# Optimization experiments

Measured on AMD Instinct MI355X. Metric: run time of the kernel, lower is better.

The kernel has to match this reference:

```python
import jax, jax.numpy as jnp
import numpy as np

N, D, F, E, K = 8192, 1024, 4096, 8, 2


def setup_inputs() -> dict:
    key = jax.random.key(0)
    ks = jax.random.split(key, 4)
    x = jax.random.normal(ks[0], (N, D), dtype=jnp.float32)
    Wg = jax.random.normal(ks[1], (D, E), dtype=jnp.float32) * 0.02
    W1 = jax.random.normal(ks[2], (E, D, F), dtype=jnp.float32) * 0.02
    b1 = jnp.zeros((E, F), dtype=jnp.float32)
    W2 = jax.random.normal(ks[3], (E, F, D), dtype=jnp.float32) * 0.02
    b2 = jnp.zeros((E, D), dtype=jnp.float32)
    return {"x": x, "Wg": Wg, "W1": W1, "b1": b1, "W2": W2, "b2": b2}


def reference(x, Wg, W1, b1, W2, b2):
    # Top-k softmax gate (TopKGate): pick K experts per token, renormalize.
    logits = x @ Wg                                        # [N, E]
    probs = jax.nn.softmax(logits, axis=-1)
    gate_vals, expert_idx = jax.lax.top_k(probs, K)        # [N, K]
    gate_w = gate_vals / jnp.sum(gate_vals, axis=-1, keepdims=True)

    # Expert FFN (dispatch/combine math): the torch code sorts tokens by expert
    # id, all-to-alls them to the owning rank, applies the local Expert MLP,
    # and combines back weighted by gate_w. The jit-friendly equivalent is to
    # compute every expert's MLP for all tokens and gather the selected rows.
    h = jax.nn.relu(jnp.einsum('nd,edf->enf', x, W1) + b1[:, None, :])  # [E, N, F]
    o = jnp.einsum('enf,efd->end', h, W2) + b2[:, None, :]               # [E, N, D]

    tok = jnp.arange(x.shape[0])
    sel = o[expert_idx, tok[:, None]]                      # [N, K, D]
    y = jnp.sum(gate_w[..., None] * sel, axis=1)           # [N, D]
    return y
```

## Files before the change

kernel.cpp:

```cpp
#include <hip/hip_runtime.h>

#define N_TOK 8192
#define DIM   1024
#define FFN   4096
#define NEXP  8
#define TOPK  2
#define NENT  (N_TOK * TOPK)
#define MAXM  20

using short8  = __attribute__((ext_vector_type(8))) short;
using floatx4 = __attribute__((ext_vector_type(4))) float;

__device__ __forceinline__ unsigned short f2bf(float f) {
    union { float f; unsigned u; } v; v.f = f;
    unsigned r = v.u + 0x7fffu + ((v.u >> 16) & 1u);
    return (unsigned short)(r >> 16);
}

__device__ __forceinline__ float bf2f(unsigned short s) {
    union { unsigned u; float f; } v; v.u = ((unsigned)s) << 16;
    return v.f;
}

#define GLOAD_LDS16(gptr, lptr) __builtin_amdgcn_global_load_lds( \
    (__attribute__((address_space(1))) void*)(void*)(gptr),       \
    (__attribute__((address_space(3))) void*)(lptr), 16, 0, 0)


__global__ __launch_bounds__(256) void transpose_cvt(const float* __restrict__ in,
                                                     unsigned short* __restrict__ out,
                                                     int R, int C) {
    __shared__ float tile[64][65];
    int e  = blockIdx.z;
    int c0 = blockIdx.x * 64;
    int r0 = blockIdx.y * 64;
    const float* inp = in + (size_t)e * R * C;
    unsigned short* outp = out + (size_t)e * R * C;
    int tid = threadIdx.x;
    int lrow = tid >> 4;
    int lc4  = (tid & 15) * 4;
#pragma unroll
    for (int i = 0; i < 4; i++) {
        int r = i * 16 + lrow;
        float4 v = *(const float4*)&inp[(size_t)(r0 + r) * C + c0 + lc4];
        tile[r][lc4 + 0] = v.x;
        tile[r][lc4 + 1] = v.y;
        tile[r][lc4 + 2] = v.z;
        tile[r][lc4 + 3] = v.w;
    }
    __syncthreads();
    int r4 = (tid & 15) * 4;
#pragma unroll
    for (int i = 0; i < 4; i++) {
        int c = i * 16 + (tid >> 4);
        ushort4 o;
        o.x = f2bf(tile[r4 + 0][c]);
        o.y = f2bf(tile[r4 + 1][c]);
        o.z = f2bf(tile[r4 + 2][c]);
        o.w = f2bf(tile[r4 + 3][c]);
        *(ushort4*)&outp[(size_t)(c0 + c) * R + r0 + r4] = o;
    }
}


__global__ __launch_bounds__(256) void gating_kernel(const float* __restrict__ x,
                                                     const float* __restrict__ wg,
                                                     unsigned short* __restrict__ xb,
                                                     int* __restrict__ topk_e,
                                                     float* __restrict__ topk_w,
                                                     int* __restrict__ counts) {
    int wave = threadIdx.x >> 6, lane = threadIdx.x & 63;
    int t = blockIdx.x * 4 + wave;
    const float* xr = x + (size_t)t * DIM;
    unsigned short* xbr = xb + (size_t)t * DIM;
    float acc[NEXP];
#pragma unroll
    for (int e = 0; e < NEXP; e++) acc[e] = 0.f;
    for (int it = 0; it < DIM / 64; it++) {
        int d = it * 64 + lane;
        float xv = xr[d];
        xbr[d] = f2bf(xv);
        const float4* wr = (const float4*)(wg + d * NEXP);
        float4 w0 = wr[0], w1 = wr[1];
        acc[0] += xv * w0.x; acc[1] += xv * w0.y; acc[2] += xv * w0.z; acc[3] += xv * w0.w;
        acc[4] += xv * w1.x; acc[5] += xv * w1.y; acc[6] += xv * w1.z; acc[7] += xv * w1.w;
    }
#pragma unroll
    for (int e = 0; e < NEXP; e++) {
#pragma unroll
        for (int off = 32; off > 0; off >>= 1) acc[e] += __shfl_xor(acc[e], off);
    }
    if (lane == 0) {
        int e1 = 0; float l1 = acc[0];
        for (int e = 1; e < NEXP; e++) if (acc[e] > l1) { l1 = acc[e]; e1 = e; }
        int e2 = -1; float l2 = -3.4e38f;
        for (int e = 0; e < NEXP; e++) if (e != e1 && acc[e] > l2) { l2 = acc[e]; e2 = e; }
        float w1v = 1.f / (1.f + expf(l2 - l1));
        topk_e[t * 2]     = e1;  topk_e[t * 2 + 1] = e2;
        topk_w[t * 2]     = w1v; topk_w[t * 2 + 1] = 1.f - w1v;
        atomicAdd(&counts[e1], 1);
        atomicAdd(&counts[e2], 1);
    }
}

__global__ __launch_bounds__(256) void scatter_kernel(const int* __restrict__ topk_e,
                                                      const float* __restrict__ topk_w,
                                                      const int* __restrict__ counts,
                                                      int* __restrict__ offs,
                                                      int* __restrict__ cursors,
                                                      int* __restrict__ entry_token,
                                                      int* __restrict__ entry_pos) {
    int off_[NEXP]; int s = 0;
#pragma unroll
    for (int e = 0; e < NEXP; e++) { off_[e] = s; s += counts[e]; }
    if (blockIdx.x == 0 && threadIdx.x == 0) {
#pragma unroll
        for (int e = 0; e < NEXP; e++) offs[e] = off_[e];
        offs[NEXP] = s;
    }
    int t = blockIdx.x * 256 + threadIdx.x;
#pragma unroll
    for (int k = 0; k < TOPK; k++) {
        int e = topk_e[t * 2 + k];
        int pos = off_[e] + atomicAdd(&cursors[e], 1);
        entry_token[pos] = t;
        entry_pos[t * 2 + k] = pos;
    }
}


__global__ __launch_bounds__(256, 3) void gemm1_kernel(
    const unsigned short* __restrict__ xb,
    const unsigned short* __restrict__ w1t,
    const float* __restrict__ b1,
    const int* __restrict__ offs,
    const int* __restrict__ entry_token,
    unsigned short* __restrict__ h)
{
    int bid   = blockIdx.x;
    int xcd   = bid & 7;
    int inner = bid >> 3;
    int gq    = inner / MAXM;
    int mt    = inner - gq * MAXM;
    int g     = gq * 8 + xcd;
    int e     = g >> 5;
    int nt    = g & 31;
    int base = offs[e];
    int cnt  = offs[e + 1] - base;
    int m0   = mt * 128;
    if (m0 >= cnt) return;
    int f0   = nt * 128;

    __shared__ unsigned short As[2][128 * 32];
    __shared__ unsigned short Bs[2][128 * 32];
    __shared__ int toks[128];

    int tid = threadIdx.x;
    if (tid < 128) {
        int r = m0 + tid;
        toks[tid] = entry_token[base + (r < cnt ? r : 0)];
    }
    __syncthreads();

    int wave = tid >> 6, lane = tid & 63;
    int wm = (wave >> 1) * 64, wn = (wave & 1) * 64;

    int lr = lane >> 2, sl = lane & 3;
    int g0 = (sl ^ ((lr >> 1) & 3)) * 8;
    const unsigned short* aG[2];
    const unsigned short* bG[2];
    int ldsOff[2];
#pragma unroll
    for (int c = 0; c < 2; c++) {
        int row = wave * 32 + c * 16 + lr;
        aG[c] = xb + (size_t)toks[row] * DIM + g0;
        bG[c] = w1t + ((size_t)e * FFN + f0 + row) * DIM + g0;
        ldsOff[c] = (wave * 32 + c * 16) * 32;
    }

    floatx4 acc[4][4];
#pragma unroll
    for (int i = 0; i < 4; i++)
#pragma unroll
        for (int j = 0; j < 4; j++) acc[i][j] = (floatx4)0.f;

    int quad = lane >> 4, rm = lane & 15;
    int slf  = (quad ^ ((rm >> 1) & 3)) * 8;
    int arow = (wm + rm) * 32;
    int brow = (wn + rm) * 32;

#pragma unroll
    for (int c = 0; c < 2; c++) {
        GLOAD_LDS16(aG[c], &As[0][ldsOff[c]]);
        GLOAD_LDS16(bG[c], &Bs[0][ldsOff[c]]);
        aG[c] += 32; bG[c] += 32;
    }

    int cur = 0;
    for (int kk = 0; kk < DIM / 32; kk++) {
        __syncthreads();
        short8 af[4], bfr[4];
#pragma unroll
        for (int mi = 0; mi < 4; mi++) af[mi] = *(const short8*)&As[cur][arow + mi * 512 + slf];
#pragma unroll
        for (int ni = 0; ni < 4; ni++) bfr[ni] = *(const short8*)&Bs[cur][brow + ni * 512 + slf];
        if (kk + 1 < DIM / 32) {
            int nxt = cur ^ 1;
#pragma unroll
            for (int c = 0; c < 2; c++) {
                GLOAD_LDS16(aG[c], &As[nxt][ldsOff[c]]);
                GLOAD_LDS16(bG[c], &Bs[nxt][ldsOff[c]]);
                aG[c] += 32; bG[c] += 32;
            }
        }
#pragma unroll
        for (int mi = 0; mi < 4; mi++)
#pragma unroll
            for (int ni = 0; ni < 4; ni++)
                acc[mi][ni] = __builtin_amdgcn_mfma_f32_16x16x32_bf16(af[mi], bfr[ni], acc[mi][ni], 0, 0, 0);
        cur ^= 1;
    }

#pragma unroll
    for (int mi = 0; mi < 4; mi++) {
        int mbase = wm + mi * 16 + quad * 4;
#pragma unroll
        for (int ni = 0; ni < 4; ni++) {
            int f = f0 + wn + ni * 16 + rm;
            float bias = b1[e * FFN + f];
            floatx4 v = acc[mi][ni];
#pragma unroll
            for (int r = 0; r < 4; r++) {
                int row = m0 + mbase + r;
                if (row < cnt) {
                    float t = v[r] + bias;
                    t = t > 0.f ? t : 0.f;
                    h[(size_t)(base + row) * FFN + f] = f2bf(t);
                }
            }
        }
    }
}


__global__ __launch_bounds__(256, 3) void gemm2_kernel(
    const unsigned short* __restrict__ h,
    const unsigned short* __restrict__ w2t,
    const float* __restrict__ b2,
    const int* __restrict__ offs,
    unsigned short* __restrict__ o)
{
    int bid  = blockIdx.x;
    int e    = bid & 7;
    int grp  = bid % (8 * MAXM);
    int mt   = grp >> 3;
    int nt   = bid / (8 * MAXM);
    int base = offs[e];
    int cnt  = offs[e + 1] - base;
    int m0   = mt * 128;
    if (m0 >= cnt) return;
    int n0   = nt * 128;

    __shared__ unsigned short As[2][128 * 32];
    __shared__ unsigned short Bs[2][128 * 32];

    int tid = threadIdx.x;
    int wave = tid >> 6, lane = tid & 63;
    int wm = (wave >> 1) * 64, wn = (wave & 1) * 64;

    int lr = lane >> 2, sl = lane & 3;
    int g0 = (sl ^ ((lr >> 1) & 3)) * 8;
    const unsigned short* aG[2];
    const unsigned short* bG[2];
    int ldsOff[2];
#pragma unroll
    for (int c = 0; c < 2; c++) {
        int row = wave * 32 + c * 16 + lr;
        aG[c] = h + (size_t)(base + m0 + row) * FFN + g0;
        bG[c] = w2t + ((size_t)e * DIM + n0 + row) * FFN + g0;
        ldsOff[c] = (wave * 32 + c * 16) * 32;
    }

    floatx4 acc[4][4];
#pragma unroll
    for (int i = 0; i < 4; i++)
#pragma unroll
        for (int j = 0; j < 4; j++) acc[i][j] = (floatx4)0.f;

    int quad = lane >> 4, rm = lane & 15;
    int slf  = (quad ^ ((rm >> 1) & 3)) * 8;
    int arow = (wm + rm) * 32;
    int brow = (wn + rm) * 32;

#pragma unroll
    for (int c = 0; c < 2; c++) {
        GLOAD_LDS16(aG[c], &As[0][ldsOff[c]]);
        GLOAD_LDS16(bG[c], &Bs[0][ldsOff[c]]);
        aG[c] += 32; bG[c] += 32;
    }

    int cur = 0;
    for (int kk = 0; kk < FFN / 32; kk++) {
        __syncthreads();
        short8 af[4], bfr[4];
#pragma unroll
        for (int mi = 0; mi < 4; mi++) af[mi] = *(const short8*)&As[cur][arow + mi * 512 + slf];
#pragma unroll
        for (int ni = 0; ni < 4; ni++) bfr[ni] = *(const short8*)&Bs[cur][brow + ni * 512 + slf];
        if (kk + 1 < FFN / 32) {
            int nxt = cur ^ 1;
#pragma unroll
            for (int c = 0; c < 2; c++) {
                GLOAD_LDS16(aG[c], &As[nxt][ldsOff[c]]);
                GLOAD_LDS16(bG[c], &Bs[nxt][ldsOff[c]]);
                aG[c] += 32; bG[c] += 32;
            }
        }
#pragma unroll
        for (int mi = 0; mi < 4; mi++)
#pragma unroll
            for (int ni = 0; ni < 4; ni++)
                acc[mi][ni] = __builtin_amdgcn_mfma_f32_16x16x32_bf16(af[mi], bfr[ni], acc[mi][ni], 0, 0, 0);
        cur ^= 1;
    }

#pragma unroll
    for (int mi = 0; mi < 4; mi++) {
        int mbase = wm + mi * 16 + quad * 4;
#pragma unroll
        for (int ni = 0; ni < 4; ni++) {
            int n = n0 + wn + ni * 16 + rm;
            float bias = b2[e * DIM + n];
            floatx4 v = acc[mi][ni];
#pragma unroll
            for (int r = 0; r < 4; r++) {
                int row = m0 + mbase + r;
                if (row < cnt)
                    o[(size_t)(base + row) * DIM + n] = f2bf(v[r] + bias);
            }
        }
    }
}


__global__ __launch_bounds__(256) void combine_kernel(const unsigned short* __restrict__ o,
                                                      const int* __restrict__ entry_pos,
                                                      const float* __restrict__ topk_w,
                                                      float* __restrict__ y) {
    int t = blockIdx.x;
    int d = threadIdx.x * 4;
    int p0 = entry_pos[t * 2], p1 = entry_pos[t * 2 + 1];
    float w0 = topk_w[t * 2], w1 = topk_w[t * 2 + 1];
    ushort4 a = *(const ushort4*)&o[(size_t)p0 * DIM + d];
    ushort4 b = *(const ushort4*)&o[(size_t)p1 * DIM + d];
    float4 r;
    r.x = w0 * bf2f(a.x) + w1 * bf2f(b.x);
    r.y = w0 * bf2f(a.y) + w1 * bf2f(b.y);
    r.z = w0 * bf2f(a.z) + w1 * bf2f(b.z);
    r.w = w0 * bf2f(a.w) + w1 * bf2f(b.w);
    *(float4*)&y[(size_t)t * DIM + d] = r;
}


extern "C" void kernel_launch(void* const* d_in, const int* in_sizes, int n_in,
                              void* d_out, int out_size, void* d_ws, size_t ws_size,
                              hipStream_t stream) {
    const float* x  = (const float*)d_in[0];
    const float* Wg = (const float*)d_in[1];
    const float* W1 = (const float*)d_in[2];
    const float* b1 = (const float*)d_in[3];
    const float* W2 = (const float*)d_in[4];
    const float* b2 = (const float*)d_in[5];
    float* y = (float*)d_out;

    char* p = (char*)d_ws;
    unsigned short* xb  = (unsigned short*)p; p += (size_t)N_TOK * DIM * 2;
    unsigned short* w1t = (unsigned short*)p; p += (size_t)NEXP * DIM * FFN * 2;
    unsigned short* w2t = (unsigned short*)p; p += (size_t)NEXP * DIM * FFN * 2;
    unsigned short* h   = (unsigned short*)p; p += (size_t)(NENT + 128) * FFN * 2;
    int*   topk_e      = (int*)p;   p += (size_t)N_TOK * TOPK * 4;
    float* topk_w      = (float*)p; p += (size_t)N_TOK * TOPK * 4;
    int*   entry_token = (int*)p;   p += (size_t)NENT * 4;
    int*   entry_pos   = (int*)p;   p += (size_t)NENT * 4;
    int*   counts      = (int*)p;   p += NEXP * 4;
    int*   cursors     = (int*)p;   p += NEXP * 4;
    int*   offs        = (int*)p;   p += (NEXP + 1) * 4;

    unsigned short* o = w1t;

    hipMemsetAsync(counts, 0, NEXP * 4 * 2, stream);

    transpose_cvt<<<dim3(FFN / 64, DIM / 64, NEXP), 256, 0, stream>>>(W1, w1t, DIM, FFN);
    transpose_cvt<<<dim3(DIM / 64, FFN / 64, NEXP), 256, 0, stream>>>(W2, w2t, FFN, DIM);
    gating_kernel<<<N_TOK / 4, 256, 0, stream>>>(x, Wg, xb, topk_e, topk_w, counts);
    scatter_kernel<<<N_TOK / 256, 256, 0, stream>>>(topk_e, topk_w, counts, offs, cursors, entry_token, entry_pos);
    gemm1_kernel<<<NEXP * MAXM * (FFN / 128), 256, 0, stream>>>(xb, w1t, b1, offs, entry_token, h);
    gemm2_kernel<<<NEXP * MAXM * (DIM / 128), 256, 0, stream>>>(h, w2t, b2, offs, o);
    combine_kernel<<<N_TOK, 256, 0, stream>>>(o, entry_pos, topk_w, y);
}
```

Before: 996.0 us.

## Fuse combine into gemm2 epilogue via atomics and merge prep kernels

The weight transposes and the gating kernel are merged into one launch, and the gating loop now uses float4 loads. The combine kernel is removed. gemm2's epilogue instead scales each row by its gate weight and atomically adds it into a zeroed fp32 output, indexed by token. This drops the bf16 intermediate o buffer, its write and read-back, and two launches, at the cost of a memset of y, scattered fp32 atomics, and non-deterministic summation order.

```diff
diff --git a/kernel.cpp b/kernel.cpp
--- a/kernel.cpp
+++ b/kernel.cpp
@@ -17,73 +17,85 @@
     return (unsigned short)(r >> 16);
 }
 
-__device__ __forceinline__ float bf2f(unsigned short s) {
-    union { unsigned u; float f; } v; v.u = ((unsigned)s) << 16;
-    return v.f;
-}
-
 #define GLOAD_LDS16(gptr, lptr) __builtin_amdgcn_global_load_lds( \
     (__attribute__((address_space(1))) void*)(void*)(gptr),       \
     (__attribute__((address_space(3))) void*)(lptr), 16, 0, 0)
 
 
-__global__ __launch_bounds__(256) void transpose_cvt(const float* __restrict__ in,
-                                                     unsigned short* __restrict__ out,
-                                                     int R, int C) {
+__global__ __launch_bounds__(256) void prep_kernel(
+    const float* __restrict__ W1, const float* __restrict__ W2,
+    unsigned short* __restrict__ w1t, unsigned short* __restrict__ w2t,
+    const float* __restrict__ x, const float* __restrict__ wg,
+    unsigned short* __restrict__ xb,
+    int* __restrict__ topk_e, float* __restrict__ topk_w,
+    int* __restrict__ counts)
+{
     __shared__ float tile[64][65];
-    int e  = blockIdx.z;
-    int c0 = blockIdx.x * 64;
-    int r0 = blockIdx.y * 64;
-    const float* inp = in + (size_t)e * R * C;
-    unsigned short* outp = out + (size_t)e * R * C;
+    int bid = blockIdx.x;
     int tid = threadIdx.x;
-    int lrow = tid >> 4;
-    int lc4  = (tid & 15) * 4;
-#pragma unroll
-    for (int i = 0; i < 4; i++) {
-        int r = i * 16 + lrow;
-        float4 v = *(const float4*)&inp[(size_t)(r0 + r) * C + c0 + lc4];
-        tile[r][lc4 + 0] = v.x;
-        tile[r][lc4 + 1] = v.y;
-        tile[r][lc4 + 2] = v.z;
-        tile[r][lc4 + 3] = v.w;
-    }
-    __syncthreads();
-    int r4 = (tid & 15) * 4;
-#pragma unroll
-    for (int i = 0; i < 4; i++) {
-        int c = i * 16 + (tid >> 4);
-        ushort4 o;
-        o.x = f2bf(tile[r4 + 0][c]);
-        o.y = f2bf(tile[r4 + 1][c]);
-        o.z = f2bf(tile[r4 + 2][c]);
-        o.w = f2bf(tile[r4 + 3][c]);
-        *(ushort4*)&outp[(size_t)(c0 + c) * R + r0 + r4] = o;
-    }
-}
-
-
-__global__ __launch_bounds__(256) void gating_kernel(const float* __restrict__ x,
-                                                     const float* __restrict__ wg,
-                                                     unsigned short* __restrict__ xb,
-                                                     int* __restrict__ topk_e,
-                                                     float* __restrict__ topk_w,
-                                                     int* __restrict__ counts) {
-    int wave = threadIdx.x >> 6, lane = threadIdx.x & 63;
-    int t = blockIdx.x * 4 + wave;
+
+    if (bid < 16384) {
+        const float* in; unsigned short* out; int R, C, e, c0, r0;
+        if (bid < 8192) {
+            in = W1; out = w1t; R = DIM; C = FFN;
+            e = bid >> 10; int b = bid & 1023;
+            c0 = (b & 63) * 64; r0 = (b >> 6) * 64;
+        } else {
+            int bb = bid - 8192;
+            in = W2; out = w2t; R = FFN; C = DIM;
+            e = bb >> 10; int b = bb & 1023;
+            c0 = (b & 15) * 64; r0 = (b >> 4) * 64;
+        }
+        const float* inp = in + (size_t)e * DIM * FFN;
+        unsigned short* outp = out + (size_t)e * DIM * FFN;
+        int lrow = tid >> 4;
+        int lc4  = (tid & 15) * 4;
+#pragma unroll
+        for (int i = 0; i < 4; i++) {
+            int r = i * 16 + lrow;
+            float4 v = *(const float4*)&inp[(size_t)(r0 + r) * C + c0 + lc4];
+            tile[r][lc4 + 0] = v.x;
+            tile[r][lc4 + 1] = v.y;
+            tile[r][lc4 + 2] = v.z;
+            tile[r][lc4 + 3] = v.w;
+        }
+        __syncthreads();
+        int r4 = (tid & 15) * 4;
+#pragma unroll
+        for (int i = 0; i < 4; i++) {
+            int c = i * 16 + (tid >> 4);
+            ushort4 o;
+            o.x = f2bf(tile[r4 + 0][c]);
+            o.y = f2bf(tile[r4 + 1][c]);
+            o.z = f2bf(tile[r4 + 2][c]);
+            o.w = f2bf(tile[r4 + 3][c]);
+            *(ushort4*)&outp[(size_t)(c0 + c) * R + r0 + r4] = o;
+        }
+        return;
+    }
+
+    int wave = tid >> 6, lane = tid & 63;
+    int t = (bid - 16384) * 4 + wave;
     const float* xr = x + (size_t)t * DIM;
     unsigned short* xbr = xb + (size_t)t * DIM;
     float acc[NEXP];
 #pragma unroll
     for (int e = 0; e < NEXP; e++) acc[e] = 0.f;
-    for (int it = 0; it < DIM / 64; it++) {
-        int d = it * 64 + lane;
-        float xv = xr[d];
-        xbr[d] = f2bf(xv);
-        const float4* wr = (const float4*)(wg + d * NEXP);
-        float4 w0 = wr[0], w1 = wr[1];
-        acc[0] += xv * w0.x; acc[1] += xv * w0.y; acc[2] += xv * w0.z; acc[3] += xv * w0.w;
-        acc[4] += xv * w1.x; acc[5] += xv * w1.y; acc[6] += xv * w1.z; acc[7] += xv * w1.w;
+    for (int it = 0; it < DIM / 256; it++) {
+        int d = it * 256 + lane * 4;
+        float4 xv = *(const float4*)&xr[d];
+        ushort4 ub;
+        ub.x = f2bf(xv.x); ub.y = f2bf(xv.y); ub.z = f2bf(xv.z); ub.w = f2bf(xv.w);
+        *(ushort4*)&xbr[d] = ub;
+        const float* wp = wg + (size_t)d * NEXP;
+#pragma unroll
+        for (int j = 0; j < 4; j++) {
+            float xj = (j == 0) ? xv.x : (j == 1) ? xv.y : (j == 2) ? xv.z : xv.w;
+            const float4* wr = (const float4*)(wp + j * NEXP);
+            float4 w0 = wr[0], w1 = wr[1];
+            acc[0] += xj * w0.x; acc[1] += xj * w0.y; acc[2] += xj * w0.z; acc[3] += xj * w0.w;
+            acc[4] += xj * w1.x; acc[5] += xj * w1.y; acc[6] += xj * w1.z; acc[7] += xj * w1.w;
+        }
     }
 #pragma unroll
     for (int e = 0; e < NEXP; e++) {
@@ -109,7 +121,7 @@
                                                       int* __restrict__ offs,
                                                       int* __restrict__ cursors,
                                                       int* __restrict__ entry_token,
-                                                      int* __restrict__ entry_pos) {
+                                                      float* __restrict__ entry_w) {
     int off_[NEXP]; int s = 0;
 #pragma unroll
     for (int e = 0; e < NEXP; e++) { off_[e] = s; s += counts[e]; }
@@ -124,7 +136,7 @@
         int e = topk_e[t * 2 + k];
         int pos = off_[e] + atomicAdd(&cursors[e], 1);
         entry_token[pos] = t;
-        entry_pos[t * 2 + k] = pos;
+        entry_w[pos] = topk_w[t * 2 + k];
     }
 }
 
@@ -248,7 +260,9 @@
     const unsigned short* __restrict__ w2t,
     const float* __restrict__ b2,
     const int* __restrict__ offs,
-    unsigned short* __restrict__ o)
+    const int* __restrict__ entry_token,
+    const float* __restrict__ entry_w,
+    float* __restrict__ y)
 {
     int bid  = blockIdx.x;
     int e    = bid & 7;
@@ -324,41 +338,27 @@
         cur ^= 1;
     }
 
+    float bs[4];
+#pragma unroll
+    for (int ni = 0; ni < 4; ni++) bs[ni] = b2[e * DIM + n0 + wn + ni * 16 + rm];
 #pragma unroll
     for (int mi = 0; mi < 4; mi++) {
         int mbase = wm + mi * 16 + quad * 4;
 #pragma unroll
-        for (int ni = 0; ni < 4; ni++) {
-            int n = n0 + wn + ni * 16 + rm;
-            float bias = b2[e * DIM + n];
-            floatx4 v = acc[mi][ni];
-#pragma unroll
-            for (int r = 0; r < 4; r++) {
-                int row = m0 + mbase + r;
-                if (row < cnt)
-                    o[(size_t)(base + row) * DIM + n] = f2bf(v[r] + bias);
+        for (int r = 0; r < 4; r++) {
+            int row = m0 + mbase + r;
+            if (row < cnt) {
+                int tok = entry_token[base + row];
+                float w = entry_w[base + row];
+                float* yr = y + (size_t)tok * DIM;
+#pragma unroll
+                for (int ni = 0; ni < 4; ni++) {
+                    int n = n0 + wn + ni * 16 + rm;
+                    atomicAdd(&yr[n], w * (acc[mi][ni][r] + bs[ni]));
+                }
             }
         }
     }
-}
-
-
-__global__ __launch_bounds__(256) void combine_kernel(const unsigned short* __restrict__ o,
-                                                      const int* __restrict__ entry_pos,
-                                                      const float* __restrict__ topk_w,
-                                                      float* __restrict__ y) {
-    int t = blockIdx.x;
-    int d = threadIdx.x * 4;
-    int p0 = entry_pos[t * 2], p1 = entry_pos[t * 2 + 1];
-    float w0 = topk_w[t * 2], w1 = topk_w[t * 2 + 1];
-    ushort4 a = *(const ushort4*)&o[(size_t)p0 * DIM + d];
-    ushort4 b = *(const ushort4*)&o[(size_t)p1 * DIM + d];
-    float4 r;
-    r.x = w0 * bf2f(a.x) + w1 * bf2f(b.x);
-    r.y = w0 * bf2f(a.y) + w1 * bf2f(b.y);
-    r.z = w0 * bf2f(a.z) + w1 * bf2f(b.z);
-    r.w = w0 * bf2f(a.w) + w1 * bf2f(b.w);
-    *(float4*)&y[(size_t)t * DIM + d] = r;
 }
 
 
@@ -381,20 +381,19 @@
     int*   topk_e      = (int*)p;   p += (size_t)N_TOK * TOPK * 4;
     float* topk_w      = (float*)p; p += (size_t)N_TOK * TOPK * 4;
     int*   entry_token = (int*)p;   p += (size_t)NENT * 4;
-    int*   entry_pos   = (int*)p;   p += (size_t)NENT * 4;
+    float* entry_w     = (float*)p; p += (size_t)NENT * 4;
     int*   counts      = (int*)p;   p += NEXP * 4;
     int*   cursors     = (int*)p;   p += NEXP * 4;
     int*   offs        = (int*)p;   p += (NEXP + 1) * 4;
 
-    unsigned short* o = w1t;
-
     hipMemsetAsync(counts, 0, NEXP * 4 * 2, stream);
-
-    transpose_cvt<<<dim3(FFN / 64, DIM / 64, NEXP), 256, 0, stream>>>(W1, w1t, DIM, FFN);
-    transpose_cvt<<<dim3(DIM / 64, FFN / 64, NEXP), 256, 0, stream>>>(W2, w2t, FFN, DIM);
-    gating_kernel<<<N_TOK / 4, 256, 0, stream>>>(x, Wg, xb, topk_e, topk_w, counts);
-    scatter_kernel<<<N_TOK / 256, 256, 0, stream>>>(topk_e, topk_w, counts, offs, cursors, entry_token, entry_pos);
+    hipMemsetAsync(y, 0, (size_t)N_TOK * DIM * 4, stream);
+
+    prep_kernel<<<16384 + N_TOK / 4, 256, 0, stream>>>(W1, W2, w1t, w2t, x, Wg, xb,
+                                                       topk_e, topk_w, counts);
+    scatter_kernel<<<N_TOK / 256, 256, 0, stream>>>(topk_e, topk_w, counts, offs,
+                                                    cursors, entry_token, entry_w);
     gemm1_kernel<<<NEXP * MAXM * (FFN / 128), 256, 0, stream>>>(xb, w1t, b1, offs, entry_token, h);
-    gemm2_kernel<<<NEXP * MAXM * (DIM / 128), 256, 0, stream>>>(h, w2t, b2, offs, o);
-    combine_kernel<<<N_TOK, 256, 0, stream>>>(o, entry_pos, topk_w, y);
-}
+    gemm2_kernel<<<NEXP * MAXM * (DIM / 128), 256, 0, stream>>>(h, w2t, b2, offs,
+                                                                entry_token, entry_w, y);
+}
```

Result: no change. 0.9995 ms (+0.4%).
